# Kernel optimization log

Measured on AMD Instinct MI355X. Metric: run time of the kernel, lower is better.

## Reference

```python
import jax, jax.numpy as jnp
from jax import lax
import numpy as np

B, T, N = 128, 4096, 32
SMOOTH = 1.0


def setup_inputs() -> dict:
    key = jax.random.key(0)
    k1, k2, k3, k4 = jax.random.split(key, 4)
    potentials = jax.random.normal(k1, (B, T, N), dtype=jnp.float32)
    y_true = jax.random.randint(k2, (B, T), 0, N)
    lengths = jax.random.randint(k3, (B,), 1, T + 1)
    transitions = jax.random.normal(k4, (N, N), dtype=jnp.float32) * 0.1
    return {"potentials": potentials, "y_true": y_true,
            "lengths": lengths, "transitions": transitions}


def crf_marginals(potentials, lengths, transitions):
    """Linear-chain CRF posterior marginals p(y_t = k | x), shape [B, T, N]."""
    Bq, Tq, Nq = potentials.shape
    lengths = lengths.astype(jnp.int32)
    # valid[t-1, b] == (t < lengths[b]) for t = 1..T-1
    valid = jnp.arange(1, Tq)[:, None] < lengths[None, :]  # [T-1, B]
    pots_t = jnp.transpose(potentials[:, 1:], (1, 0, 2))    # [T-1, B, N]

    # forward recursion (carry alpha unchanged past sequence end)
    def fwd_step(alpha_prev, inp):
        pot_t, v = inp
        new = jax.nn.logsumexp(alpha_prev[:, :, None] + transitions[None], axis=1) + pot_t
        alpha = jnp.where(v[:, None], new, alpha_prev)
        return alpha, alpha

    alpha0 = potentials[:, 0]
    _, alphas_rest = lax.scan(fwd_step, alpha0, (pots_t, valid))
    alphas = jnp.concatenate([alpha0[None], alphas_rest], axis=0)  # [T, B, N]

    # backward recursion (beta = 0 at/after the last valid position)
    def bwd_step(beta_next, inp):
        pot_next, v = inp  # pot_next is potentials at t+1; v == (t+1 < length)
        new = jax.nn.logsumexp(transitions[None] + (pot_next + beta_next)[:, None, :], axis=2)
        beta = jnp.where(v[:, None], new, jnp.zeros_like(new))
        return beta, beta

    beta_last = jnp.zeros((Bq, Nq), dtype=potentials.dtype)
    _, betas_rest = lax.scan(bwd_step, beta_last, (pots_t, valid), reverse=True)
    betas = jnp.concatenate([betas_rest, beta_last[None]], axis=0)  # [T, B, N]

    # since alpha is frozen past the end, alphas[-1] == alpha_{length-1}
    logZ = jax.nn.logsumexp(alphas[-1], axis=-1)  # [B]
    log_marg = alphas + betas - logZ[None, :, None]
    return jnp.exp(jnp.transpose(log_marg, (1, 0, 2)))  # [B, T, N]


def reference(potentials, y_true, lengths, transitions):
    probs = crf_marginals(potentials, lengths, transitions)
    num_tags = probs.shape[-1]
    y_oh = jax.nn.one_hot(y_true.astype(jnp.int32), num_tags, dtype=probs.dtype)
    Tq = probs.shape[1]
    mask_btn = (jnp.arange(Tq)[None, :] < lengths.astype(jnp.int32)[:, None]
                ).astype(probs.dtype)[:, :, None]
    y_m = y_oh * mask_btn
    p_m = probs * mask_btn
    inter = jnp.sum(y_m * p_m, axis=(1, 2))
    sums = jnp.sum(y_m, axis=(1, 2)) + jnp.sum(p_m, axis=(1, 2))
    dice = (2.0 * inter + SMOOTH) / (sums + SMOOTH)
    return 1.0 - dice
```

## Files before the change

kernel.cpp:

```cpp
#include <hip/hip_runtime.h>
#include <hip/hip_bf16.h>

#define Bq 128
#define Tq 4096
#define Nq 32
#define SEGL 128
#define NSEG 32
#define BURN 25
#define TRIPB 24
#define TRIP 152
#define UNR 8
#define NBLK 19
#define LOG2E 1.4426950408889634f

typedef float v2f __attribute__((ext_vector_type(2)));
typedef float v4f __attribute__((ext_vector_type(4)));
typedef unsigned short u16;

__device__ __forceinline__ u16 f2bf(float f) {
  unsigned u = __float_as_uint(f);
  u = u + 0x7fffu + ((u >> 16) & 1u);
  return (u16)(u >> 16);
}

extern "C" __global__ void __launch_bounds__(64, 4)
crf_chain_kernel(const float* __restrict__ pot, const int* __restrict__ lengths,
                 const float* __restrict__ trans,
                 u16* __restrict__ eaF, u16* __restrict__ eaB) {
  __shared__ v4f sbuf4[16];
  float* sbuf = (float*)sbuf4;
  const int tid = threadIdx.x;
  const int j = tid & 31;
  const int half = tid >> 5;
  const int b = blockIdx.x >> 5;
  const int s = blockIdx.x & 31;
  const int len = lengths[b];
  const int sL = s * SEGL;
  if (sL >= len) return;
  const int lenm1 = len - 1;
  const int tend = min(sL + SEGL, len);
  const int end = tend - 1;
  const int t1 = min(lenm1, end + BURN);

  const int dir = half ? -1 : 1;
  const int cst  = half ? (end + BURN) : ((s == 0) ? (1 - TRIPB) : (sL - BURN + 1));
  const int skip = half ? (end + BURN - t1) : ((s == 0) ? TRIPB : 0);
  const int wlo = sL;
  const int whi = half ? min(end, t1) : end;
  const unsigned uspan = (unsigned)(whi - wlo);

  v2f eT2[16];
#pragma unroll
  for (int k = 0; k < 16; ++k) {
    const int i0 = 2 * k, i1 = 2 * k + 1;
    float ta = half ? trans[j * Nq + i0] : trans[i0 * Nq + j];
    float tb = half ? trans[j * Nq + i1] : trans[i1 * Nq + j];
    eT2[k].x = exp2f(ta * LOG2E);
    eT2[k].y = exp2f(tb * LOG2E);
  }

  const float* pb = pot + (size_t)b * Tq * Nq;
  const int rinit = half ? 0 : ((s == 0) ? 0 : sL - BURN);
  float raw = half ? 1.0f : exp2f(pb[rinit * Nq + j] * LOG2E);

  u16* outp = (half ? eaB : eaF) + (size_t)b * Tq * Nq + j
              + (ptrdiff_t)(cst - half) * Nq;

  int c = cst;
  float pn[UNR];
#pragma unroll
  for (int k = 0; k < UNR; ++k) {
    int cc = min(max(c + dir * k, 0), lenm1);
    pn[k] = pb[cc * Nq + j];
  }

  int gb = 0;
#pragma unroll 1
  for (int blk = 0; blk < NBLK; ++blk) {
    float pc[UNR];
#pragma unroll
    for (int k = 0; k < UNR; ++k) pc[k] = pn[k];
#pragma unroll
    for (int k = 0; k < UNR; ++k) {
      int cc = min(max(c + dir * (k + UNR), 0), lenm1);
      pn[k] = pb[cc * Nq + j];
    }
#pragma unroll
    for (int k = 0; k < UNR; ++k) {
      float epot = exp2f(pc[k] * LOG2E);
      float pre = half ? raw * epot : raw;
      sbuf[tid] = pre;
      v4f B0 = sbuf4[(half << 3) + 0];
      v4f B1 = sbuf4[(half << 3) + 1];
      v4f B2 = sbuf4[(half << 3) + 2];
      v4f B3 = sbuf4[(half << 3) + 3];
      v4f B4 = sbuf4[(half << 3) + 4];
      v4f B5 = sbuf4[(half << 3) + 5];
      v4f B6 = sbuf4[(half << 3) + 6];
      v4f B7 = sbuf4[(half << 3) + 7];
      int eb = __float_as_int(B0.x) & 0x7f800000;
      float corr = __int_as_float(0x7f000000 - eb);
      v2f p, a0, a1, a2, a3;
      p.x = B0.x; p.y = B0.y; a0 = p * eT2[0];
      p.x = B0.z; p.y = B0.w; a1 = p * eT2[1];
      p.x = B1.x; p.y = B1.y; a2 = p * eT2[2];
      p.x = B1.z; p.y = B1.w; a3 = p * eT2[3];
      p.x = B2.x; p.y = B2.y; a0 += p * eT2[4];
      p.x = B2.z; p.y = B2.w; a1 += p * eT2[5];
      p.x = B3.x; p.y = B3.y; a2 += p * eT2[6];
      p.x = B3.z; p.y = B3.w; a3 += p * eT2[7];
      p.x = B4.x; p.y = B4.y; a0 += p * eT2[8];
      p.x = B4.z; p.y = B4.w; a1 += p * eT2[9];
      p.x = B5.x; p.y = B5.y; a2 += p * eT2[10];
      p.x = B5.z; p.y = B5.w; a3 += p * eT2[11];
      p.x = B6.x; p.y = B6.y; a0 += p * eT2[12];
      p.x = B6.z; p.y = B6.w; a1 += p * eT2[13];
      p.x = B7.x; p.y = B7.y; a2 += p * eT2[14];
      p.x = B7.z; p.y = B7.w; a3 += p * eT2[15];
      v2f asum = (a0 + a1) + (a2 + a3);
      float hsum = asum.x + asum.y;
      float qc = corr * (half ? 1.0f : epot);
      float nr = hsum * qc;
      raw = ((gb + k) >= skip) ? nr : raw;
      int r = c - half;
      if ((unsigned)(r - wlo) <= uspan) *outp = f2bf(raw);
      outp += dir * Nq;
      c += dir;
    }
    gb += UNR;
  }
}

extern "C" __global__ void __launch_bounds__(1024)
dice_kernel(const u16* __restrict__ eaF, const u16* __restrict__ eaB,
            const int* __restrict__ y, const int* __restrict__ lengths,
            float* __restrict__ out) {
  const int b = blockIdx.x;
  const int tid = threadIdx.x;
  const int len = lengths[b];
  const size_t base = (size_t)b * Tq;
  float I = 0.f;
#pragma unroll
  for (int q = 0; q < Tq / 1024; ++q) {
    int t = tid + q * 1024;
    if (t < len) {
      const u16* ar = eaF + (base + t) * Nq;
      const u16* br = eaB + (base + t) * Nq;
      const uint4* a4 = (const uint4*)ar;
      const uint4* b4 = (const uint4*)br;
      float c0 = 0.f, c1 = 0.f, c2 = 0.f, c3 = 0.f;
#pragma unroll
      for (int w = 0; w < 4; ++w) {
        uint4 ua = a4[w], ub = b4[w];
        c0 = fmaf(__uint_as_float(ua.x << 16), __uint_as_float(ub.x << 16), c0);
        c1 = fmaf(__uint_as_float(ua.x & 0xffff0000u), __uint_as_float(ub.x & 0xffff0000u), c1);
        c2 = fmaf(__uint_as_float(ua.y << 16), __uint_as_float(ub.y << 16), c2);
        c3 = fmaf(__uint_as_float(ua.y & 0xffff0000u), __uint_as_float(ub.y & 0xffff0000u), c3);
        c0 = fmaf(__uint_as_float(ua.z << 16), __uint_as_float(ub.z << 16), c0);
        c1 = fmaf(__uint_as_float(ua.z & 0xffff0000u), __uint_as_float(ub.z & 0xffff0000u), c1);
        c2 = fmaf(__uint_as_float(ua.w << 16), __uint_as_float(ub.w << 16), c2);
        c3 = fmaf(__uint_as_float(ua.w & 0xffff0000u), __uint_as_float(ub.w & 0xffff0000u), c3);
      }
      float v = (c0 + c1) + (c2 + c3);
      int yt = y[base + t];
      float ay = __uint_as_float(((unsigned)ar[yt]) << 16);
      float by = __uint_as_float(((unsigned)br[yt]) << 16);
      I += (ay * by) / v;
    }
  }
#pragma unroll
  for (int m = 1; m < 64; m <<= 1) I += __shfl_xor(I, m);
  __shared__ float sI[16];
  if ((tid & 63) == 0) sI[tid >> 6] = I;
  __syncthreads();
  if (tid == 0) {
    float It = 0.f;
#pragma unroll
    for (int k = 0; k < 16; ++k) It += sI[k];
    float dice = (2.f * It + 1.f) / (2.f * (float)len + 1.f);
    out[b] = 1.f - dice;
  }
}

extern "C" void kernel_launch(void* const* d_in, const int* in_sizes, int n_in,
                              void* d_out, int out_size, void* d_ws, size_t ws_size,
                              hipStream_t stream) {
  const float* pot = (const float*)d_in[0];
  const int* y_true = (const int*)d_in[1];
  const int* lengths = (const int*)d_in[2];
  const float* trans = (const float*)d_in[3];
  float* out = (float*)d_out;

  char* ws = (char*)d_ws;
  const size_t n_elems = (size_t)Bq * Tq * Nq;
  u16* eaF = (u16*)ws;
  u16* eaB = (u16*)(ws + n_elems * 2);

  crf_chain_kernel<<<Bq * NSEG, 64, 0, stream>>>(pot, lengths, trans, eaF, eaB);
  dice_kernel<<<Bq, 1024, 0, stream>>>(eaF, eaB, y_true, lengths, out);
}
```

Before: 173.3 us.

## Split each CRF chain across 16 lanes with bf16 LDS exchange and split dice

Each forward or backward chain segment now runs on 16 threads, each owning two tags, and four chains are packed per 64-lane wave in 256-thread blocks. The state exchanged through shared memory is packed as bf16 pairs, which halves LDS traffic. The burn-in length drops from 25 to 16 steps and the unroll factor from 8 to 4. The dice reduction is split into 16 blocks per batch element that use atomics, followed by a tiny final kernel. The aims are to raise occupancy, cut per-step LDS reads and shorten the serial chain, at the cost of bf16 rounding inside the recursion, a shorter burn-in that may affect accuracy, and an extra launch.

```diff
diff --git a/kernel.cpp b/kernel.cpp
--- a/kernel.cpp
+++ b/kernel.cpp
@@ -6,180 +6,189 @@
 #define Nq 32
 #define SEGL 128
 #define NSEG 32
-#define BURN 25
-#define TRIPB 24
-#define TRIP 152
-#define UNR 8
-#define NBLK 19
+#define BURN 16
+#define TRIPB 15
+#define UNR 4
+#define NBLK 36
 #define LOG2E 1.4426950408889634f
 
 typedef float v2f __attribute__((ext_vector_type(2)));
-typedef float v4f __attribute__((ext_vector_type(4)));
 typedef unsigned short u16;
 
-__device__ __forceinline__ u16 f2bf(float f) {
-  unsigned u = __float_as_uint(f);
-  u = u + 0x7fffu + ((u >> 16) & 1u);
-  return (u16)(u >> 16);
-}
-
-extern "C" __global__ void __launch_bounds__(64, 4)
+__device__ __forceinline__ unsigned pack_bf16(float f0, float f1) {
+  unsigned u0 = __float_as_uint(f0);
+  unsigned u1 = __float_as_uint(f1);
+  u0 = u0 + 0x7fffu + ((u0 >> 16) & 1u);
+  u1 = u1 + 0x7fffu + ((u1 >> 16) & 1u);
+  return (u0 >> 16) | (u1 & 0xffff0000u);
+}
+
+extern "C" __global__ void __launch_bounds__(256)
 crf_chain_kernel(const float* __restrict__ pot, const int* __restrict__ lengths,
                  const float* __restrict__ trans,
-                 u16* __restrict__ eaF, u16* __restrict__ eaB) {
-  __shared__ v4f sbuf4[16];
-  float* sbuf = (float*)sbuf4;
+                 u16* __restrict__ eaF, u16* __restrict__ eaB,
+                 float* __restrict__ iacc) {
+  __shared__ unsigned xbuf[16][16];
   const int tid = threadIdx.x;
-  const int j = tid & 31;
-  const int half = tid >> 5;
-  const int b = blockIdx.x >> 5;
-  const int s = blockIdx.x & 31;
+  if (blockIdx.x == 0 && tid < Bq) iacc[tid] = 0.f;
+
+  const int cslot = tid >> 4;
+  const int sub = tid & 15;
+  const int oc = sub * 2;
+  const int cid = blockIdx.x * 16 + cslot;
+  const int b = cid >> 6;
+  const int dir = (cid >> 5) & 1;
+  const int s = cid & 31;
   const int len = lengths[b];
   const int sL = s * SEGL;
-  if (sL >= len) return;
+  const bool active = (sL < len);
+  if (__ballot(active) == 0ull) return;
+
   const int lenm1 = len - 1;
   const int tend = min(sL + SEGL, len);
   const int end = tend - 1;
   const int t1 = min(lenm1, end + BURN);
-
-  const int dir = half ? -1 : 1;
-  const int cst  = half ? (end + BURN) : ((s == 0) ? (1 - TRIPB) : (sL - BURN + 1));
-  const int skip = half ? (end + BURN - t1) : ((s == 0) ? TRIPB : 0);
+  const int dstep = dir ? -1 : 1;
+  const int cst = dir ? (end + BURN) : ((s == 0) ? (1 - TRIPB) : (sL - BURN + 1));
+  const int skip = dir ? (end + BURN - t1) : ((s == 0) ? TRIPB : 0);
   const int wlo = sL;
-  const int whi = half ? min(end, t1) : end;
+  const int whi = dir ? min(end, t1) : end;
   const unsigned uspan = (unsigned)(whi - wlo);
 
-  v2f eT2[16];
+  v2f eTa[16], eTb[16];
 #pragma unroll
   for (int k = 0; k < 16; ++k) {
     const int i0 = 2 * k, i1 = 2 * k + 1;
-    float ta = half ? trans[j * Nq + i0] : trans[i0 * Nq + j];
-    float tb = half ? trans[j * Nq + i1] : trans[i1 * Nq + j];
-    eT2[k].x = exp2f(ta * LOG2E);
-    eT2[k].y = exp2f(tb * LOG2E);
+    float a0 = dir ? trans[oc * Nq + i0] : trans[i0 * Nq + oc];
+    float a1 = dir ? trans[oc * Nq + i1] : trans[i1 * Nq + oc];
+    float b0 = dir ? trans[(oc + 1) * Nq + i0] : trans[i0 * Nq + oc + 1];
+    float b1 = dir ? trans[(oc + 1) * Nq + i1] : trans[i1 * Nq + oc + 1];
+    v2f ea, eb;
+    ea.x = exp2f(a0 * LOG2E); ea.y = exp2f(a1 * LOG2E);
+    eb.x = exp2f(b0 * LOG2E); eb.y = exp2f(b1 * LOG2E);
+    eTa[k] = ea; eTb[k] = eb;
   }
 
   const float* pb = pot + (size_t)b * Tq * Nq;
-  const int rinit = half ? 0 : ((s == 0) ? 0 : sL - BURN);
-  float raw = half ? 1.0f : exp2f(pb[rinit * Nq + j] * LOG2E);
-
-  u16* outp = (half ? eaB : eaF) + (size_t)b * Tq * Nq + j
-              + (ptrdiff_t)(cst - half) * Nq;
-
-  int c = cst;
-  float pn[UNR];
+  float raw0, raw1;
+  if (dir) { raw0 = 1.f; raw1 = 1.f; }
+  else {
+    const int rinit = (s == 0) ? 0 : (sL - BURN);
+    raw0 = exp2f(pb[rinit * Nq + oc] * LOG2E);
+    raw1 = exp2f(pb[rinit * Nq + oc + 1] * LOG2E);
+  }
+  u16* outbase = (dir ? eaB : eaF) + ((size_t)b * Tq) * Nq + oc;
+  if (!dir) { if (active && s == 0) *(unsigned*)outbase = pack_bf16(raw0, raw1); }
+  else      { if (active && t1 <= end) *(unsigned*)(outbase + (size_t)t1 * Nq) = pack_bf16(1.f, 1.f); }
+
+  int cb = cst;
+  int r = cst - dir;
+  u16* outp = outbase + (ptrdiff_t)r * Nq;
+  v2f pn[UNR];
 #pragma unroll
   for (int k = 0; k < UNR; ++k) {
-    int cc = min(max(c + dir * k, 0), lenm1);
-    pn[k] = pb[cc * Nq + j];
-  }
-
-  int gb = 0;
+    int cc = min(max(cb + dstep * k, 0), lenm1);
+    pn[k] = *(const v2f*)(pb + cc * Nq + oc);
+  }
+
+  int g0 = 0;
 #pragma unroll 1
   for (int blk = 0; blk < NBLK; ++blk) {
-    float pc[UNR];
+    v2f pc[UNR];
 #pragma unroll
     for (int k = 0; k < UNR; ++k) pc[k] = pn[k];
 #pragma unroll
     for (int k = 0; k < UNR; ++k) {
-      int cc = min(max(c + dir * (k + UNR), 0), lenm1);
-      pn[k] = pb[cc * Nq + j];
+      int cc = min(max(cb + dstep * (k + UNR), 0), lenm1);
+      pn[k] = *(const v2f*)(pb + cc * Nq + oc);
     }
 #pragma unroll
     for (int k = 0; k < UNR; ++k) {
-      float epot = exp2f(pc[k] * LOG2E);
-      float pre = half ? raw * epot : raw;
-      sbuf[tid] = pre;
-      v4f B0 = sbuf4[(half << 3) + 0];
-      v4f B1 = sbuf4[(half << 3) + 1];
-      v4f B2 = sbuf4[(half << 3) + 2];
-      v4f B3 = sbuf4[(half << 3) + 3];
-      v4f B4 = sbuf4[(half << 3) + 4];
-      v4f B5 = sbuf4[(half << 3) + 5];
-      v4f B6 = sbuf4[(half << 3) + 6];
-      v4f B7 = sbuf4[(half << 3) + 7];
-      int eb = __float_as_int(B0.x) & 0x7f800000;
+      float ep0 = exp2f(pc[k].x * LOG2E);
+      float ep1 = exp2f(pc[k].y * LOG2E);
+      float w0 = dir ? raw0 * ep0 : raw0;
+      float w1 = dir ? raw1 * ep1 : raw1;
+      xbuf[cslot][sub] = pack_bf16(w0, w1);
+      const uint4* xb4 = (const uint4*)&xbuf[cslot][0];
+      uint4 B0 = xb4[0], B1 = xb4[1], B2 = xb4[2], B3 = xb4[3];
+      int eb = (int)((B0.x << 16) & 0x7f800000u);
       float corr = __int_as_float(0x7f000000 - eb);
-      v2f p, a0, a1, a2, a3;
-      p.x = B0.x; p.y = B0.y; a0 = p * eT2[0];
-      p.x = B0.z; p.y = B0.w; a1 = p * eT2[1];
-      p.x = B1.x; p.y = B1.y; a2 = p * eT2[2];
-      p.x = B1.z; p.y = B1.w; a3 = p * eT2[3];
-      p.x = B2.x; p.y = B2.y; a0 += p * eT2[4];
-      p.x = B2.z; p.y = B2.w; a1 += p * eT2[5];
-      p.x = B3.x; p.y = B3.y; a2 += p * eT2[6];
-      p.x = B3.z; p.y = B3.w; a3 += p * eT2[7];
-      p.x = B4.x; p.y = B4.y; a0 += p * eT2[8];
-      p.x = B4.z; p.y = B4.w; a1 += p * eT2[9];
-      p.x = B5.x; p.y = B5.y; a2 += p * eT2[10];
-      p.x = B5.z; p.y = B5.w; a3 += p * eT2[11];
-      p.x = B6.x; p.y = B6.y; a0 += p * eT2[12];
-      p.x = B6.z; p.y = B6.w; a1 += p * eT2[13];
-      p.x = B7.x; p.y = B7.y; a2 += p * eT2[14];
-      p.x = B7.z; p.y = B7.w; a3 += p * eT2[15];
-      v2f asum = (a0 + a1) + (a2 + a3);
-      float hsum = asum.x + asum.y;
-      float qc = corr * (half ? 1.0f : epot);
-      float nr = hsum * qc;
-      raw = ((gb + k) >= skip) ? nr : raw;
-      int r = c - half;
-      if ((unsigned)(r - wlo) <= uspan) *outp = f2bf(raw);
-      outp += dir * Nq;
-      c += dir;
+      v2f a0, a1, a2, a3, d0, d1, d2, d3;
+      a0 = 0.f; a1 = 0.f; a2 = 0.f; a3 = 0.f;
+      d0 = 0.f; d1 = 0.f; d2 = 0.f; d3 = 0.f;
+#define ACC(dw, p, A, D) { v2f xp; \
+      xp.x = __uint_as_float((dw) << 16); \
+      xp.y = __uint_as_float((dw) & 0xffff0000u); \
+      A += xp * eTa[p]; D += xp * eTb[p]; }
+      ACC(B0.x, 0, a0, d0) ACC(B0.y, 1, a1, d1) ACC(B0.z, 2, a2, d2) ACC(B0.w, 3, a3, d3)
+      ACC(B1.x, 4, a0, d0) ACC(B1.y, 5, a1, d1) ACC(B1.z, 6, a2, d2) ACC(B1.w, 7, a3, d3)
+      ACC(B2.x, 8, a0, d0) ACC(B2.y, 9, a1, d1) ACC(B2.z,10, a2, d2) ACC(B2.w,11, a3, d3)
+      ACC(B3.x,12, a0, d0) ACC(B3.y,13, a1, d1) ACC(B3.z,14, a2, d2) ACC(B3.w,15, a3, d3)
+#undef ACC
+      v2f sa = (a0 + a1) + (a2 + a3);
+      v2f sd = (d0 + d1) + (d2 + d3);
+      float s0 = sa.x + sa.y;
+      float s1 = sd.x + sd.y;
+      float n0 = s0 * corr * (dir ? 1.f : ep0);
+      float n1 = s1 * corr * (dir ? 1.f : ep1);
+      const bool upd = (g0 + k) >= skip;
+      raw0 = upd ? n0 : raw0;
+      raw1 = upd ? n1 : raw1;
+      if (active && (unsigned)(r - wlo) <= uspan) *(unsigned*)outp = pack_bf16(raw0, raw1);
+      outp += dstep * Nq;
+      r += dstep;
     }
-    gb += UNR;
-  }
-}
-
-extern "C" __global__ void __launch_bounds__(1024)
+    cb += dstep * UNR;
+    g0 += UNR;
+  }
+}
+
+extern "C" __global__ void __launch_bounds__(256)
 dice_kernel(const u16* __restrict__ eaF, const u16* __restrict__ eaB,
             const int* __restrict__ y, const int* __restrict__ lengths,
-            float* __restrict__ out) {
-  const int b = blockIdx.x;
-  const int tid = threadIdx.x;
+            float* __restrict__ iacc) {
+  const int b = blockIdx.x >> 4;
+  const int q = blockIdx.x & 15;
   const int len = lengths[b];
-  const size_t base = (size_t)b * Tq;
+  if (q * 256 >= len) return;
+  const int t = q * 256 + threadIdx.x;
   float I = 0.f;
-#pragma unroll
-  for (int q = 0; q < Tq / 1024; ++q) {
-    int t = tid + q * 1024;
-    if (t < len) {
-      const u16* ar = eaF + (base + t) * Nq;
-      const u16* br = eaB + (base + t) * Nq;
-      const uint4* a4 = (const uint4*)ar;
-      const uint4* b4 = (const uint4*)br;
-      float c0 = 0.f, c1 = 0.f, c2 = 0.f, c3 = 0.f;
-#pragma unroll
-      for (int w = 0; w < 4; ++w) {
-        uint4 ua = a4[w], ub = b4[w];
-        c0 = fmaf(__uint_as_float(ua.x << 16), __uint_as_float(ub.x << 16), c0);
-        c1 = fmaf(__uint_as_float(ua.x & 0xffff0000u), __uint_as_float(ub.x & 0xffff0000u), c1);
-        c2 = fmaf(__uint_as_float(ua.y << 16), __uint_as_float(ub.y << 16), c2);
-        c3 = fmaf(__uint_as_float(ua.y & 0xffff0000u), __uint_as_float(ub.y & 0xffff0000u), c3);
-        c0 = fmaf(__uint_as_float(ua.z << 16), __uint_as_float(ub.z << 16), c0);
-        c1 = fmaf(__uint_as_float(ua.z & 0xffff0000u), __uint_as_float(ub.z & 0xffff0000u), c1);
-        c2 = fmaf(__uint_as_float(ua.w << 16), __uint_as_float(ub.w << 16), c2);
-        c3 = fmaf(__uint_as_float(ua.w & 0xffff0000u), __uint_as_float(ub.w & 0xffff0000u), c3);
-      }
-      float v = (c0 + c1) + (c2 + c3);
-      int yt = y[base + t];
-      float ay = __uint_as_float(((unsigned)ar[yt]) << 16);
-      float by = __uint_as_float(((unsigned)br[yt]) << 16);
-      I += (ay * by) / v;
+  if (t < len) {
+    const size_t base = ((size_t)b * Tq + t) * Nq;
+    const uint4* a4 = (const uint4*)(eaF + base);
+    const uint4* b4 = (const uint4*)(eaB + base);
+    float c0 = 0.f, c1 = 0.f, c2 = 0.f, c3 = 0.f;
+#pragma unroll
+    for (int w = 0; w < 4; ++w) {
+      uint4 ua = a4[w], ub = b4[w];
+      c0 = fmaf(__uint_as_float(ua.x << 16), __uint_as_float(ub.x << 16), c0);
+      c1 = fmaf(__uint_as_float(ua.x & 0xffff0000u), __uint_as_float(ub.x & 0xffff0000u), c1);
+      c2 = fmaf(__uint_as_float(ua.y << 16), __uint_as_float(ub.y << 16), c2);
+      c3 = fmaf(__uint_as_float(ua.y & 0xffff0000u), __uint_as_float(ub.y & 0xffff0000u), c3);
+      c0 = fmaf(__uint_as_float(ua.z << 16), __uint_as_float(ub.z << 16), c0);
+      c1 = fmaf(__uint_as_float(ua.z & 0xffff0000u), __uint_as_float(ub.z & 0xffff0000u), c1);
+      c2 = fmaf(__uint_as_float(ua.w << 16), __uint_as_float(ub.w << 16), c2);
+      c3 = fmaf(__uint_as_float(ua.w & 0xffff0000u), __uint_as_float(ub.w & 0xffff0000u), c3);
     }
+    float v = (c0 + c1) + (c2 + c3);
+    int yt = y[(size_t)b * Tq + t];
+    float ay = __uint_as_float(((unsigned)eaF[base + yt]) << 16);
+    float by = __uint_as_float(((unsigned)eaB[base + yt]) << 16);
+    I = (ay * by) / v;
   }
 #pragma unroll
   for (int m = 1; m < 64; m <<= 1) I += __shfl_xor(I, m);
-  __shared__ float sI[16];
-  if ((tid & 63) == 0) sI[tid >> 6] = I;
+  __shared__ float sI[4];
+  if ((threadIdx.x & 63) == 0) sI[threadIdx.x >> 6] = I;
   __syncthreads();
-  if (tid == 0) {
-    float It = 0.f;
-#pragma unroll
-    for (int k = 0; k < 16; ++k) It += sI[k];
-    float dice = (2.f * It + 1.f) / (2.f * (float)len + 1.f);
-    out[b] = 1.f - dice;
-  }
+  if (threadIdx.x == 0) atomicAdd(&iacc[b], sI[0] + sI[1] + sI[2] + sI[3]);
+}
+
+extern "C" __global__ void final_kernel(const float* __restrict__ iacc,
+                                        const int* __restrict__ lengths,
+                                        float* __restrict__ out) {
+  const int b = threadIdx.x;
+  if (b < Bq) out[b] = 1.f - (2.f * iacc[b] + 1.f) / (2.f * (float)lengths[b] + 1.f);
 }
 
 extern "C" void kernel_launch(void* const* d_in, const int* in_sizes, int n_in,
@@ -195,7 +204,9 @@
   const size_t n_elems = (size_t)Bq * Tq * Nq;
   u16* eaF = (u16*)ws;
   u16* eaB = (u16*)(ws + n_elems * 2);
-
-  crf_chain_kernel<<<Bq * NSEG, 64, 0, stream>>>(pot, lengths, trans, eaF, eaB);
-  dice_kernel<<<Bq, 1024, 0, stream>>>(eaF, eaB, y_true, lengths, out);
-}
+  float* iacc = (float*)(ws + n_elems * 4);
+
+  crf_chain_kernel<<<512, 256, 0, stream>>>(pot, lengths, trans, eaF, eaB, iacc);
+  dice_kernel<<<Bq * 16, 256, 0, stream>>>(eaF, eaB, y_true, lengths, iacc);
+  final_kernel<<<1, 128, 0, stream>>>(iacc, lengths, out);
+}
```

Measured after the change: 185.7 us. 1.07x slower.
